# Optimization experiments

Measured on AMD Instinct MI355X. Metric: run time of the kernel, lower is better.

Reference implementation:

```python
import jax, jax.numpy as jnp
import numpy as np
from jax import lax

B, C, H, W = 16, 64, 64, 64
K = 3                  # kernel_size
D_IN = C * K           # moe input dim = 192
D_OUT = 128            # out_channels
N_EXP = 8
TOP_K = 2
N_SHARED = 1


def setup_inputs() -> dict:
    key = jax.random.key(0)
    ks = jax.random.split(key, 7)
    x = jax.random.normal(ks[0], (B, C, H, W), dtype=jnp.float32)
    # depthwise conv: groups=C, each input channel -> K output channels
    conv_w = jax.random.normal(ks[1], (D_IN, 1, K, K), dtype=jnp.float32) * 0.1
    router_w = jax.random.normal(ks[2], (D_IN, N_EXP), dtype=jnp.float32) * 0.05
    w_experts = jax.random.normal(ks[3], (N_EXP, D_IN, D_OUT), dtype=jnp.float32) * 0.05
    b_experts = jnp.zeros((N_EXP, D_OUT), dtype=jnp.float32)
    w_shared = jax.random.normal(ks[4], (N_SHARED, D_IN, D_OUT), dtype=jnp.float32) * 0.05
    b_shared = jnp.zeros((N_SHARED, D_OUT), dtype=jnp.float32)
    return {"x": x, "conv_w": conv_w, "router_w": router_w,
            "w_experts": w_experts, "b_experts": b_experts,
            "w_shared": w_shared, "b_shared": b_shared}


def _moe_conv2d(x, conv_w, router_w, w_experts, b_experts, w_shared, b_shared):
    pad = K // 2
    # depthwise conv (B,C,H,W) -> (B, C*K, H, W)
    x_conv = lax.conv_general_dilated(
        x, conv_w, window_strides=(1, 1), padding=[(pad, pad), (pad, pad)],
        feature_group_count=C, dimension_numbers=("NCHW", "OIHW", "NCHW"))
    # flatten to token stream (B*H*W, D_IN)
    tokens = x_conv.transpose(0, 2, 3, 1).reshape(-1, D_IN)
    # router: softmax probs, top-k gating renormalized over selected experts
    logits = tokens @ router_w                       # (T, E)
    probs = jax.nn.softmax(logits, axis=-1)
    top_v, top_i = lax.top_k(probs, TOP_K)           # (T, k)
    gates = top_v / jnp.sum(top_v, axis=-1, keepdims=True)
    # all-expert outputs then gather the selected k per token
    expert_out = jnp.einsum("ti,eio->teo", tokens, w_experts) + b_experts  # (T, E, O)
    sel = jnp.take_along_axis(expert_out, top_i[:, :, None], axis=1)       # (T, k, O)
    y_flat = jnp.einsum("tk,tko->to", gates, sel)
    # shared experts applied to every token
    shared = jnp.einsum("ti,sio->tso", tokens, w_shared) + b_shared        # (T, S, O)
    y_flat = y_flat + jnp.sum(shared, axis=1)
    # back to feature map (B, O, H, W)
    return y_flat.reshape(B, H, W, D_OUT).transpose(0, 3, 1, 2)


def reference(x, conv_w, router_w, w_experts, b_experts, w_shared, b_shared):
    return _moe_conv2d(x, conv_w, router_w, w_experts, b_experts, w_shared, b_shared)
```

## Files before the change

kernel.cpp:

```cpp
#include <hip/hip_runtime.h>
#include <math.h>

#define BB   16
#define CC   64
#define DIN  192
#define DOUT 128
#define NEXP 8
#define NMAT 9
#define NTOK 65536
#define CAP  65568
#define SLABROWS 65552

#define TOKSTRIDE 200
#define HALFSTRIDE 104
#define LOGSTRIDE 9
#define CSTRIDE 136

typedef short bf16x8 __attribute__((ext_vector_type(8)));
typedef float f32x4  __attribute__((ext_vector_type(4)));

#define WS_TOK   0u
#define WS_WT    25165824u
#define WS_CNT   25608192u
#define WS_RT    25608256u
#define WS_RG    27706432u
#define WS_SLAB  29804608u
#define WS_TOTAL  63367232u
#define WS_TOTAL3 80148544u
#define LPHALF 524288

__device__ __forceinline__ unsigned short f2bf(float f) {
    union { float f; unsigned u; } v; v.f = f;
    unsigned u = v.u;
    u += 0x7fffu + ((u >> 16) & 1u);
    return (unsigned short)(u >> 16);
}
__device__ __forceinline__ float bf2f(unsigned short s) {
    union { unsigned u; float f; } v; v.u = ((unsigned)s) << 16;
    return v.f;
}

__global__ __launch_bounds__(256)
void k1a_conv(const float* __restrict__ x,
              const float* __restrict__ conv_w,
              const float* __restrict__ router_w,
              unsigned short* __restrict__ tokbuf,
              float* __restrict__ lpart,
              int* __restrict__ cnt)
{
    __shared__ __attribute__((aligned(16))) unsigned short tokbf[64 * HALFSTRIDE];
    __shared__ float logits[64 * LOGSTRIDE];

    const int tid   = threadIdx.x;
    const int bid   = blockIdx.x;
    const int bh    = bid >> 1;
    const int chalf = bid & 1;
    const int b     = bh >> 6;
    const int h     = bh & 63;

    if (bid == 0 && tid < 16) cnt[tid] = 0;
    for (int idx = tid; idx < 64 * LOGSTRIDE; idx += 256) logits[idx] = 0.f;
    __syncthreads();

    const int   h0  = (h > 0)  ? (h - 1) : 0;
    const int   h2  = (h < 63) ? (h + 1) : 63;
    const float mh0 = (h > 0)  ? 1.f : 0.f;
    const float mh2 = (h < 63) ? 1.f : 0.f;

    const int w = tid & 63;
    const int q = __builtin_amdgcn_readfirstlane(tid >> 6);

    const int   wm  = (w == 0)  ? 0  : (w - 1);
    const int   wp  = (w == 63) ? 63 : (w + 1);
    const float mwm = (w == 0)  ? 0.f : 1.f;
    const float mwp = (w == 63) ? 0.f : 1.f;

    float lacc[8];
    #pragma unroll
    for (int e = 0; e < 8; ++e) lacc[e] = 0.f;

    const float* xb = x + (size_t)b * CC * 4096;

    #pragma unroll 2
    for (int i = 0; i < 8; ++i) {
        const int cl = q * 8 + i;
        const int c  = chalf * 32 + cl;
        const float* xc = xb + (size_t)c * 4096;
        const float* r0 = xc + h0 * 64;
        const float* r1 = xc + h  * 64;
        const float* r2 = xc + h2 * 64;
        float x00 = r0[wm], x01 = r0[w], x02 = r0[wp];
        float x10 = r1[wm], x11 = r1[w], x12 = r1[wp];
        float x20 = r2[wm], x21 = r2[w], x22 = r2[wp];
        x00 *= mh0 * mwm; x01 *= mh0; x02 *= mh0 * mwp;
        x10 *= mwm;                    x12 *= mwp;
        x20 *= mh2 * mwm; x21 *= mh2; x22 *= mh2 * mwp;

        #pragma unroll
        for (int j = 0; j < 3; ++j) {
            const int fl = 3 * cl + j;
            const int f  = chalf * 96 + fl;
            const float* w9 = conv_w + f * 9;
            float acc = x00 * w9[0] + x01 * w9[1] + x02 * w9[2]
                      + x10 * w9[3] + x11 * w9[4] + x12 * w9[5]
                      + x20 * w9[6] + x21 * w9[7] + x22 * w9[8];
            tokbf[w * HALFSTRIDE + fl] = f2bf(acc);
            const float* rwf = router_w + f * 8;
            #pragma unroll
            for (int e = 0; e < 8; ++e) lacc[e] += acc * rwf[e];
        }
    }

    #pragma unroll
    for (int e = 0; e < 8; ++e)
        atomicAdd(&logits[w * LOGSTRIDE + e], lacc[e]);
    __syncthreads();

    for (int idx = tid; idx < 512; idx += 256) {
        int wtok = idx >> 3, e = idx & 7;
        lpart[(size_t)chalf * LPHALF + ((size_t)bh * 64 + wtok) * 8 + e] =
            logits[wtok * LOGSTRIDE + e];
    }
    for (int idx = tid; idx < 768; idx += 256) {
        int row = idx / 12, seg = idx - row * 12;
        *(bf16x8*)(tokbuf + (size_t)(bh * 64 + row) * 192 + chalf * 96 + seg * 8) =
            *(const bf16x8*)(tokbf + row * HALFSTRIDE + seg * 8);
    }
}

__global__ __launch_bounds__(256)
void k1b_route(const float* __restrict__ lpart,
               int* __restrict__ cnt,
               int* __restrict__ rowtok, float* __restrict__ rowgate,
               const float* __restrict__ w_experts,
               const float* __restrict__ w_shared,
               unsigned short* __restrict__ wt)
{
    __shared__ int lcnt[8];
    __shared__ int lbase[8];

    const int tid = threadIdx.x;
    const int blk = blockIdx.x;
    const int t   = blk * 256 + tid;

    if (tid < 8) lcnt[tid] = 0;
    __syncthreads();

    const float* p0 = lpart + (size_t)t * 8;
    const float* p1 = lpart + LPHALF + (size_t)t * 8;
    float l[8];
    #pragma unroll
    for (int e = 0; e < 8; ++e) l[e] = p0[e] + p1[e];

    int e0 = 0; float l0 = l[0];
    #pragma unroll
    for (int e = 1; e < 8; ++e) if (l[e] > l0) { l0 = l[e]; e0 = e; }
    int e1 = -1; float l1 = -INFINITY;
    #pragma unroll
    for (int e = 0; e < 8; ++e) {
        if (e == e0) continue;
        if (l[e] > l1) { l1 = l[e]; e1 = e; }
    }
    float g0 = 1.f / (1.f + expf(l1 - l0));
    float g1 = 1.f - g0;

    int r0 = atomicAdd(&lcnt[e0], 1);
    int r1 = atomicAdd(&lcnt[e1], 1);
    __syncthreads();
    if (tid < 8) lbase[tid] = atomicAdd(&cnt[tid], lcnt[tid]);
    __syncthreads();

    int p0i = e0 * CAP + lbase[e0] + r0;
    int p1i = e1 * CAP + lbase[e1] + r1;
    rowtok[p0i]  = t;
    rowgate[p0i] = g0;
    rowtok[p1i]  = t | (1 << 20);
    rowgate[p1i] = g1;

    {
        int base = blk * 864;
        for (int q = 0; q < 4; ++q) {
            int idx = base + q * 256 + tid;
            if (idx < 221184 && (q * 256 + tid) < 864) {
                int e = idx / 24576, rem = idx - e * 24576;
                int n = rem / DIN,  k  = rem - n * DIN;
                const float* src = (e < 8) ? (w_experts + (size_t)e * DIN * DOUT)
                                           : w_shared;
                wt[idx] = f2bf(src[k * DOUT + n]);
            }
        }
    }
}

__global__ __launch_bounds__(256)
void k4_all(const unsigned short* __restrict__ tokbuf,
            const unsigned short* __restrict__ wt,
            const float* __restrict__ b_experts,
            const float* __restrict__ b_shared,
            const int* __restrict__ cnt,
            const int* __restrict__ rowtok, const float* __restrict__ rowgate,
            unsigned short* __restrict__ slab)
{
    __shared__ __attribute__((aligned(16))) unsigned short atile[2][16 * TOKSTRIDE];
    __shared__ __attribute__((aligned(16))) unsigned short ctile[2][16 * CSTRIDE];
    __shared__ int   stok[2][16];
    __shared__ float sgate[2][16];

    const int tid  = threadIdx.x;
    int e, jb, jstep;
    if (blockIdx.x < 2048) { e = blockIdx.x >> 8; jb = blockIdx.x & 255; jstep = 256; }
    else                   { e = 8; jb = blockIdx.x - 2048; jstep = 1024; }
    const bool dense = (e == 8);

    const int wave = tid >> 6;
    const int lane = tid & 63;
    const int m16  = lane & 15, quad = lane >> 4;
    const int o0   = (wave * 2 + 0) * 16 + m16;
    const int o1   = (wave * 2 + 1) * 16 + m16;

    const unsigned short* wb = wt + (size_t)e * DOUT * DIN;
    bf16x8 bfr0[6], bfr1[6];
    #pragma unroll
    for (int ks = 0; ks < 6; ++ks) {
        bfr0[ks] = *(const bf16x8*)(wb + (size_t)o0 * DIN + ks * 32 + quad * 8);
        bfr1[ks] = *(const bf16x8*)(wb + (size_t)o1 * DIN + ks * 32 + quad * 8);
    }
    const float be0 = dense ? b_shared[o0] : b_experts[e * DOUT + o0];
    const float be1 = dense ? b_shared[o1] : b_experts[e * DOUT + o1];

    const int cnt_e  = dense ? NTOK : cnt[e];
    const int ntiles = (cnt_e + 15) >> 4;
    const int*   rt = rowtok  + e * CAP;
    const float* rg = rowgate + e * CAP;

    const int r0i = tid / 24,         s0i = tid - r0i * 24;
    const int r1i = (tid + 256) / 24, s1i = (tid + 256) - r1i * 24;
    const bool has1 = (tid + 256) < 384;

    #define FETCH_RAW(r) (dense ? ((r) | (2 << 20)) : (((r) < cnt_e) ? rt[r] : NTOK))
    #define FETCH_G(r)   (dense ? 1.f : (((r) < cnt_e) ? rg[r] : 0.f))

    if (jb < ntiles) {
        int base = jb * 16;
        if (tid < 16) {
            stok[0][tid]  = FETCH_RAW(base + tid);
            sgate[0][tid] = FETCH_G(base + tid);
        }
        {
            int rawa = FETCH_RAW(base + r0i);
            *(bf16x8*)&atile[0][r0i * TOKSTRIDE + s0i * 8] =
                *(const bf16x8*)(tokbuf + (size_t)(rawa & 0x1FFFF) * 192 + s0i * 8);
            if (has1) {
                int rawb = FETCH_RAW(base + r1i);
                *(bf16x8*)&atile[0][r1i * TOKSTRIDE + s1i * 8] =
                    *(const bf16x8*)(tokbuf + (size_t)(rawb & 0x1FFFF) * 192 + s1i * 8);
            }
        }
    }
    __syncthreads();

    int buf = 0;
    for (int j = jb; j < ntiles; j += jstep, buf ^= 1) {
        const int jn = j + jstep;
        const bool more = (jn < ntiles);

        bf16x8 nx0 = {0,0,0,0,0,0,0,0}, nx1 = {0,0,0,0,0,0,0,0};
        int nmt = NTOK; float nmg = 0.f;
        if (more) {
            int base = jn * 16;
            if (tid < 16) { nmt = FETCH_RAW(base + tid); nmg = FETCH_G(base + tid); }
            int rawa = FETCH_RAW(base + r0i);
            nx0 = *(const bf16x8*)(tokbuf + (size_t)(rawa & 0x1FFFF) * 192 + s0i * 8);
            if (has1) {
                int rawb = FETCH_RAW(base + r1i);
                nx1 = *(const bf16x8*)(tokbuf + (size_t)(rawb & 0x1FFFF) * 192 + s1i * 8);
            }
        }

        bf16x8 a[6];
        #pragma unroll
        for (int ks = 0; ks < 6; ++ks)
            a[ks] = *(const bf16x8*)&atile[buf][m16 * TOKSTRIDE + ks * 32 + quad * 8];

        f32x4 acc0 = {0.f, 0.f, 0.f, 0.f};
        f32x4 acc1 = {0.f, 0.f, 0.f, 0.f};
        #pragma unroll
        for (int ks = 0; ks < 6; ++ks) {
            acc0 = __builtin_amdgcn_mfma_f32_16x16x32_bf16(a[ks], bfr0[ks], acc0, 0, 0, 0);
            acc1 = __builtin_amdgcn_mfma_f32_16x16x32_bf16(a[ks], bfr1[ks], acc1, 0, 0, 0);
        }

        #pragma unroll
        for (int i = 0; i < 4; ++i) {
            int   row = quad * 4 + i;
            float g   = sgate[buf][row];
            ctile[buf][row * CSTRIDE + o0] = f2bf(g * (acc0[i] + be0));
            ctile[buf][row * CSTRIDE + o1] = f2bf(g * (acc1[i] + be1));
        }

        if (more) {
            if (tid < 16) { stok[buf ^ 1][tid] = nmt; sgate[buf ^ 1][tid] = nmg; }
            *(bf16x8*)&atile[buf ^ 1][r0i * TOKSTRIDE + s0i * 8] = nx0;
            if (has1) *(bf16x8*)&atile[buf ^ 1][r1i * TOKSTRIDE + s1i * 8] = nx1;
        }
        __syncthreads();

        {
            int row = tid >> 4, chk = tid & 15;
            int raw = stok[buf][row];
            int t    = raw & 0x1FFFF;
            int slot = raw >> 20;
            *(bf16x8*)(slab + (size_t)slot * SLABROWS * DOUT
                            + (size_t)t * DOUT + chk * 8) =
                *(const bf16x8*)&ctile[buf][row * CSTRIDE + chk * 8];
        }
    }
    #undef FETCH_RAW
    #undef FETCH_G
}

__global__ __launch_bounds__(256)
void k3_combine(const unsigned short* __restrict__ slab,
                float* __restrict__ out)
{
    __shared__ float out_lds[32 * 129];

    const int tid = threadIdx.x;
    const int bid = blockIdx.x;
    const int bh  = bid >> 1;
    const int wh  = bid & 1;
    const int b   = bh >> 6;
    const int h   = bh & 63;
    const int t0  = bh * 64 + wh * 32;

    const unsigned short* s0 = slab;
    const unsigned short* s1 = slab + (size_t)SLABROWS * DOUT;
    const unsigned short* s2 = slab + (size_t)2 * SLABROWS * DOUT;

    #pragma unroll
    for (int it = 0; it < 2; ++it) {
        int idx = it * 256 + tid;
        int tl = idx >> 4, chk = idx & 15;
        size_t gt = (size_t)t0 + tl;
        bf16x8 v0 = *(const bf16x8*)(s0 + gt * DOUT + chk * 8);
        bf16x8 v1 = *(const bf16x8*)(s1 + gt * DOUT + chk * 8);
        bf16x8 v2 = *(const bf16x8*)(s2 + gt * DOUT + chk * 8);
        float* dst = &out_lds[tl * 129 + chk * 8];
        #pragma unroll
        for (int q = 0; q < 8; ++q)
            dst[q] = bf2f((unsigned short)v0[q]) + bf2f((unsigned short)v1[q])
                   + bf2f((unsigned short)v2[q]);
    }
    __syncthreads();

    float* outp = out + ((size_t)b * DOUT) * 4096 + h * 64 + wh * 32;
    for (int idx = tid; idx < 32 * DOUT; idx += 256) {
        int wloc = idx & 31, o = idx >> 5;
        outp[(size_t)o * 4096 + wloc] = out_lds[wloc * 129 + o];
    }
}

__global__ __launch_bounds__(256)
void k3_shared(const unsigned short* __restrict__ tokbuf,
               const unsigned short* __restrict__ wt,
               const unsigned short* __restrict__ slab,
               const float* __restrict__ b_shared,
               float* __restrict__ out)
{
    __shared__ float out_lds[32 * 129];

    const int tid  = threadIdx.x;
    const int bid  = blockIdx.x;
    const int bh   = bid >> 1;
    const int wh   = bid & 1;
    const int b    = bh >> 6;
    const int h    = bh & 63;
    const int wave = tid >> 6, lane = tid & 63;
    const int mt   = wave >> 1, nh = wave & 1;
    const int m16  = lane & 15, quad = lane >> 4;
    const int t0   = bh * 64 + wh * 32;

    bf16x8 pv0[2], pv1[2];
    {
        const unsigned short* s0 = slab;
        const unsigned short* s1 = slab + (size_t)SLABROWS * DOUT;
        #pragma unroll
        for (int it = 0; it < 2; ++it) {
            int idx = it * 256 + tid;
            int tl = idx >> 4, chk = idx & 15;
            size_t gt = (size_t)t0 + tl;
            pv0[it] = *(const bf16x8*)(s0 + gt * DOUT + chk * 8);
            pv1[it] = *(const bf16x8*)(s1 + gt * DOUT + chk * 8);
        }
    }

    const unsigned short* ap =
        tokbuf + (size_t)(t0 + mt * 16 + m16) * 192 + quad * 8;
    bf16x8 a[6];
    #pragma unroll
    for (int ks = 0; ks < 6; ++ks) a[ks] = *(const bf16x8*)(ap + ks * 32);

    const unsigned short* wsh = wt + (size_t)8 * DOUT * DIN;

    bf16x8 bcur[6], bnxt[6];
    {
        int o = (nh * 4 + 0) * 16 + m16;
        const unsigned short* bp = wsh + (size_t)o * DIN + quad * 8;
        #pragma unroll
        for (int ks = 0; ks < 6; ++ks) bcur[ks] = *(const bf16x8*)(bp + ks * 32);
    }
    #pragma unroll
    for (int nb2 = 0; nb2 < 4; ++nb2) {
        if (nb2 < 3) {
            int on = (nh * 4 + nb2 + 1) * 16 + m16;
            const unsigned short* bp = wsh + (size_t)on * DIN + quad * 8;
            #pragma unroll
            for (int ks = 0; ks < 6; ++ks) bnxt[ks] = *(const bf16x8*)(bp + ks * 32);
        }
        int o = (nh * 4 + nb2) * 16 + m16;
        f32x4 acc = {0.f, 0.f, 0.f, 0.f};
        #pragma unroll
        for (int ks = 0; ks < 6; ++ks)
            acc = __builtin_amdgcn_mfma_f32_16x16x32_bf16(a[ks], bcur[ks], acc, 0, 0, 0);
        float bs = b_shared[o];
        #pragma unroll
        for (int i = 0; i < 4; ++i) {
            int tloc = mt * 16 + quad * 4 + i;
            out_lds[tloc * 129 + o] = acc[i] + bs;
        }
        #pragma unroll
        for (int ks = 0; ks < 6; ++ks) bcur[ks] = bnxt[ks];
    }
    __syncthreads();

    #pragma unroll
    for (int it = 0; it < 2; ++it) {
        int idx = it * 256 + tid;
        int tl = idx >> 4, chk = idx & 15;
        float* dst = &out_lds[tl * 129 + chk * 8];
        #pragma unroll
        for (int q = 0; q < 8; ++q)
            dst[q] += bf2f((unsigned short)pv0[it][q])
                    + bf2f((unsigned short)pv1[it][q]);
    }
    __syncthreads();

    float* outp = out + ((size_t)b * DOUT) * 4096 + h * 64 + wh * 32;
    for (int idx = tid; idx < 32 * DOUT; idx += 256) {
        int wloc = idx & 31, o = idx >> 5;
        outp[(size_t)o * 4096 + wloc] = out_lds[wloc * 129 + o];
    }
}

#define OUTSTRIDE 129
#define MAXROWS 320
#define MAXTILES 20

__global__ __launch_bounds__(256)
void moe_conv2d_mfma(const float* __restrict__ x,
                     const float* __restrict__ conv_w,
                     const float* __restrict__ router_w,
                     const unsigned short* __restrict__ wt,
                     const float* __restrict__ b_experts,
                     const float* __restrict__ b_shared,
                     float* __restrict__ out)
{
    __shared__ __attribute__((aligned(16))) unsigned short tokbf[64 * TOKSTRIDE];
    __shared__ float out_lds[64 * OUTSTRIDE];
    __shared__ float rw[DIN * NEXP];
    __shared__ float logits[64 * LOGSTRIDE];
    __shared__ float sg0[64], sg1[64];
    __shared__ int   se0[64], se1[64];
    __shared__ int   rowtok[MAXROWS];
    __shared__ float rowgate[MAXROWS];
    __shared__ int   cbuf[NMAT];
    __shared__ int   tilexp[MAXTILES], tilebase[MAXTILES];
    __shared__ int   ntiles_s;

    const int tid = threadIdx.x;
    const int bh  = blockIdx.x;
    const int b   = bh >> 6;
    const int h   = bh & 63;

    for (int idx = tid; idx < DIN * NEXP; idx += 256) rw[idx] = router_w[idx];
    for (int idx = tid; idx < 64 * LOGSTRIDE; idx += 256) logits[idx] = 0.f;
    __syncthreads();
    {
        const int w  = tid & 63;
        const int fq = tid >> 6;
        float lacc[8];
        #pragma unroll
        for (int e = 0; e < 8; ++e) lacc[e] = 0.f;
        for (int i = 0; i < 48; ++i) {
            int f = i * 4 + fq;
            int c = f / 3;
            const float* wp    = conv_w + f * 9;
            const float* xbase = x + ((size_t)(b * 64 + c) * 64) * 64;
            float acc = 0.f;
            #pragma unroll
            for (int kh = 0; kh < 3; ++kh) {
                int hh = h + kh - 1;
                if (hh < 0 || hh > 63) continue;
                const float* xrow = xbase + hh * 64;
                #pragma unroll
                for (int kw = 0; kw < 3; ++kw) {
                    int ww = w + kw - 1;
                    if (ww < 0 || ww > 63) continue;
                    acc += xrow[ww] * wp[kh * 3 + kw];
                }
            }
            tokbf[w * TOKSTRIDE + f] = f2bf(acc);
            const float* rwf = rw + f * 8;
            #pragma unroll
            for (int e = 0; e < 8; ++e) lacc[e] += acc * rwf[e];
        }
        #pragma unroll
        for (int e = 0; e < 8; ++e)
            atomicAdd(&logits[w * LOGSTRIDE + e], lacc[e]);
    }
    __syncthreads();
    if (tid < 64) {
        int w = tid;
        float l[8];
        #pragma unroll
        for (int e = 0; e < 8; ++e) l[e] = logits[w * LOGSTRIDE + e];
        int e0 = 0; float l0 = l[0];
        #pragma unroll
        for (int e = 1; e < 8; ++e) if (l[e] > l0) { l0 = l[e]; e0 = e; }
        int e1 = -1; float l1 = -INFINITY;
        #pragma unroll
        for (int e = 0; e < 8; ++e) {
            if (e == e0) continue;
            if (l[e] > l1) { l1 = l[e]; e1 = e; }
        }
        float g0 = 1.f / (1.f + expf(l1 - l0));
        sg0[w] = g0; sg1[w] = 1.f - g0;
        se0[w] = e0; se1[w] = e1;
    }
    __syncthreads();
    for (int idx = tid; idx < 64 * DOUT; idx += 256) {
        int t = idx >> 7, o = idx & 127;
        out_lds[t * OUTSTRIDE + o] = b_shared[o]
            + sg0[t] * b_experts[se0[t] * DOUT + o]
            + sg1[t] * b_experts[se1[t] * DOUT + o];
    }
    if (tid < 8) {
        int c = 0;
        for (int t = 0; t < 64; ++t) c += (se0[t] == tid) + (se1[t] == tid);
        cbuf[tid] = c;
    } else if (tid == 8) cbuf[8] = 64;
    __syncthreads();
    if (tid < NMAT) {
        int e = tid;
        int start = 0, tb = 0;
        for (int e2 = 0; e2 < e; ++e2) {
            int ce = cbuf[e2];
            int tl = (ce + 15) >> 4;
            start += tl << 4; tb += tl;
        }
        int ce = cbuf[e];
        int tl = (ce + 15) >> 4;
        for (int j = 0; j < tl; ++j) { tilexp[tb + j] = e; tilebase[tb + j] = start + (j << 4); }
        if (e == 8) ntiles_s = tb + tl;
        int j = 0;
        if (e < 8) {
            for (int t = 0; t < 64; ++t) {
                if (se0[t] == e) { rowtok[start + j] = t; rowgate[start + j] = sg0[t]; ++j; }
                if (se1[t] == e) { rowtok[start + j] = t; rowgate[start + j] = sg1[t]; ++j; }
            }
        } else {
            for (int t = 0; t < 64; ++t) { rowtok[start + j] = t; rowgate[start + j] = 1.f; ++j; }
        }
        for (; j < (tl << 4); ++j) { rowtok[start + j] = 0; rowgate[start + j] = 0.f; }
    }
    __syncthreads();
    {
        const int wave = tid >> 6;
        const int lane = tid & 63;
        const int m16  = lane & 15;
        const int quad = lane >> 4;
        const int nt   = ntiles_s;
        for (int ti = wave; ti < nt; ti += 4) {
            int e    = tilexp[ti];
            int base = tilebase[ti];
            int tA = rowtok[base + m16];
            bf16x8 a[6];
            #pragma unroll
            for (int ks = 0; ks < 6; ++ks)
                a[ks] = *(const bf16x8*)(tokbf + tA * TOKSTRIDE + ks * 32 + quad * 8);
            int st[4]; float sgt[4];
            #pragma unroll
            for (int i2 = 0; i2 < 4; ++i2) {
                int r = base + quad * 4 + i2;
                st[i2] = rowtok[r]; sgt[i2] = rowgate[r];
            }
            const unsigned short* we = wt + (size_t)e * DOUT * DIN;
            for (int n = 0; n < 8; ++n) {
                const unsigned short* wp = we + (size_t)(n * 16 + m16) * DIN + quad * 8;
                f32x4 acc = {0.f, 0.f, 0.f, 0.f};
                #pragma unroll
                for (int ks = 0; ks < 6; ++ks) {
                    bf16x8 bfr2 = *(const bf16x8*)(wp + ks * 32);
                    acc = __builtin_amdgcn_mfma_f32_16x16x32_bf16(a[ks], bfr2, acc, 0, 0, 0);
                }
                int ncol = n * 16 + m16;
                #pragma unroll
                for (int i2 = 0; i2 < 4; ++i2)
                    atomicAdd(&out_lds[st[i2] * OUTSTRIDE + ncol], sgt[i2] * acc[i2]);
            }
        }
    }
    __syncthreads();
    {
        float* outp = out + (((size_t)b * DOUT) * 64 + h) * 64;
        for (int idx = tid; idx < 64 * DOUT; idx += 256) {
            int w = idx & 63, o = idx >> 6;
            outp[(size_t)o * 4096 + w] = out_lds[w * OUTSTRIDE + o];
        }
    }
}

__global__ __launch_bounds__(256)
void prep_weights_only(const float* __restrict__ w_experts,
                       const float* __restrict__ w_shared,
                       unsigned short* __restrict__ wt)
{
    int e = blockIdx.x;
    const float* src = (e < 8) ? (w_experts + (size_t)e * DIN * DOUT) : w_shared;
    unsigned short* dst = wt + (size_t)e * DOUT * DIN;
    for (int idx = threadIdx.x; idx < DOUT * DIN; idx += 256) {
        int n = idx / DIN, k = idx - n * DIN;
        dst[idx] = f2bf(src[k * DOUT + n]);
    }
}

extern "C" void kernel_launch(void* const* d_in, const int* in_sizes, int n_in,
                              void* d_out, int out_size, void* d_ws, size_t ws_size,
                              hipStream_t stream)
{
    const float* x         = (const float*)d_in[0];
    const float* conv_w    = (const float*)d_in[1];
    const float* router_w  = (const float*)d_in[2];
    const float* w_experts = (const float*)d_in[3];
    const float* b_experts = (const float*)d_in[4];
    const float* w_shared  = (const float*)d_in[5];
    const float* b_shared  = (const float*)d_in[6];
    float* out = (float*)d_out;
    char* ws = (char*)d_ws;

    if (ws_size >= WS_TOTAL) {
        unsigned short* tokbuf  = (unsigned short*)(ws + WS_TOK);
        unsigned short* wt      = (unsigned short*)(ws + WS_WT);
        int*            cnt     = (int*)(ws + WS_CNT);
        int*            rowtok  = (int*)(ws + WS_RT);
        float*          rowgate = (float*)(ws + WS_RG);
        unsigned short* slab    = (unsigned short*)(ws + WS_SLAB);
        float*          lpart   = (float*)(ws + WS_SLAB);

        k1a_conv<<<dim3(2048), dim3(256), 0, stream>>>(
            x, conv_w, router_w, tokbuf, lpart, cnt);
        k1b_route<<<dim3(256), dim3(256), 0, stream>>>(
            lpart, cnt, rowtok, rowgate, w_experts, w_shared, wt);
        if (ws_size >= WS_TOTAL3) {
            k4_all<<<dim3(3072), dim3(256), 0, stream>>>(
                tokbuf, wt, b_experts, b_shared, cnt, rowtok, rowgate, slab);
            k3_combine<<<dim3(2048), dim3(256), 0, stream>>>(slab, out);
        } else {
            k4_all<<<dim3(2048), dim3(256), 0, stream>>>(
                tokbuf, wt, b_experts, b_shared, cnt, rowtok, rowgate, slab);
            k3_shared<<<dim3(2048), dim3(256), 0, stream>>>(
                tokbuf, wt, slab, b_shared, out);
        }
    } else {
        unsigned short* wt = (unsigned short*)ws;
        prep_weights_only<<<dim3(NMAT), dim3(256), 0, stream>>>(w_experts, w_shared, wt);
        moe_conv2d_mfma<<<dim3(1024), dim3(256), 0, stream>>>(
            x, conv_w, router_w, wt, b_experts, b_shared, out);
    }
}
```

Baseline: 165.4 us.

## Fuse routing and weight conversion into conv kernel, one block per row

Each conv block now handles all 64 channels of one image row instead of half, so full router logits are available locally and top-2 routing plus row-slot assignment happen in the same kernel. This removes the separate routing kernel, the partial-logit round trip through global memory and one launch, and the weight transpose/bf16 conversion is spread across the conv blocks. The counter reset moves to a memset. In exchange the grid is halved, so each block does twice the conv work with a larger LDS tile, which lowers parallelism.

```diff
diff --git a/kernel.cpp b/kernel.cpp
--- a/kernel.cpp
+++ b/kernel.cpp
@@ -12,7 +12,6 @@
 #define SLABROWS 65552
 
 #define TOKSTRIDE 200
-#define HALFSTRIDE 104
 #define LOGSTRIDE 9
 #define CSTRIDE 136
 
@@ -27,7 +26,6 @@
 #define WS_SLAB  29804608u
 #define WS_TOTAL  63367232u
 #define WS_TOTAL3 80148544u
-#define LPHALF 524288
 
 __device__ __forceinline__ unsigned short f2bf(float f) {
     union { float f; unsigned u; } v; v.f = f;
@@ -44,23 +42,37 @@
 void k1a_conv(const float* __restrict__ x,
               const float* __restrict__ conv_w,
               const float* __restrict__ router_w,
+              const float* __restrict__ w_experts,
+              const float* __restrict__ w_shared,
               unsigned short* __restrict__ tokbuf,
-              float* __restrict__ lpart,
-              int* __restrict__ cnt)
+              unsigned short* __restrict__ wt,
+              int* __restrict__ cnt,
+              int* __restrict__ rowtok, float* __restrict__ rowgate)
 {
-    __shared__ __attribute__((aligned(16))) unsigned short tokbf[64 * HALFSTRIDE];
+    __shared__ __attribute__((aligned(16))) unsigned short tokbf[64 * TOKSTRIDE];
     __shared__ float logits[64 * LOGSTRIDE];
-
-    const int tid   = threadIdx.x;
-    const int bid   = blockIdx.x;
-    const int bh    = bid >> 1;
-    const int chalf = bid & 1;
-    const int b     = bh >> 6;
-    const int h     = bh & 63;
-
-    if (bid == 0 && tid < 16) cnt[tid] = 0;
+    __shared__ int lcnt[8];
+    __shared__ int lbase[8];
+
+    const int tid = threadIdx.x;
+    const int bh  = blockIdx.x;
+    const int b   = bh >> 6;
+    const int h   = bh & 63;
+
     for (int idx = tid; idx < 64 * LOGSTRIDE; idx += 256) logits[idx] = 0.f;
-    __syncthreads();
+    if (tid < 8) lcnt[tid] = 0;
+    __syncthreads();
+
+    {
+        int idx = bh * 216 + tid;
+        if (tid < 216) {
+            int e = idx / 24576, rem = idx - e * 24576;
+            int n = rem / DIN,  k  = rem - n * DIN;
+            const float* src = (e < 8) ? (w_experts + (size_t)e * DIN * DOUT)
+                                       : w_shared;
+            wt[idx] = f2bf(src[k * DOUT + n]);
+        }
+    }
 
     const int   h0  = (h > 0)  ? (h - 1) : 0;
     const int   h2  = (h < 63) ? (h + 1) : 63;
@@ -82,9 +94,8 @@
     const float* xb = x + (size_t)b * CC * 4096;
 
     #pragma unroll 2
-    for (int i = 0; i < 8; ++i) {
-        const int cl = q * 8 + i;
-        const int c  = chalf * 32 + cl;
+    for (int i = 0; i < 16; ++i) {
+        const int c = q * 16 + i;
         const float* xc = xb + (size_t)c * 4096;
         const float* r0 = xc + h0 * 64;
         const float* r1 = xc + h  * 64;
@@ -98,14 +109,13 @@
 
         #pragma unroll
         for (int j = 0; j < 3; ++j) {
-            const int fl = 3 * cl + j;
-            const int f  = chalf * 96 + fl;
-            const float* w9 = conv_w + f * 9;
+            const int f = 3 * c + j;
+            const float* w9  = conv_w + f * 9;
+            const float* rwf = router_w + f * 8;
             float acc = x00 * w9[0] + x01 * w9[1] + x02 * w9[2]
                       + x10 * w9[3] + x11 * w9[4] + x12 * w9[5]
                       + x20 * w9[6] + x21 * w9[7] + x22 * w9[8];
-            tokbf[w * HALFSTRIDE + fl] = f2bf(acc);
-            const float* rwf = router_w + f * 8;
+            tokbf[w * TOKSTRIDE + f] = f2bf(acc);
             #pragma unroll
             for (int e = 0; e < 8; ++e) lacc[e] += acc * rwf[e];
         }
@@ -116,79 +126,43 @@
         atomicAdd(&logits[w * LOGSTRIDE + e], lacc[e]);
     __syncthreads();
 
-    for (int idx = tid; idx < 512; idx += 256) {
-        int wtok = idx >> 3, e = idx & 7;
-        lpart[(size_t)chalf * LPHALF + ((size_t)bh * 64 + wtok) * 8 + e] =
-            logits[wtok * LOGSTRIDE + e];
-    }
-    for (int idx = tid; idx < 768; idx += 256) {
-        int row = idx / 12, seg = idx - row * 12;
-        *(bf16x8*)(tokbuf + (size_t)(bh * 64 + row) * 192 + chalf * 96 + seg * 8) =
-            *(const bf16x8*)(tokbf + row * HALFSTRIDE + seg * 8);
-    }
-}
-
-__global__ __launch_bounds__(256)
-void k1b_route(const float* __restrict__ lpart,
-               int* __restrict__ cnt,
-               int* __restrict__ rowtok, float* __restrict__ rowgate,
-               const float* __restrict__ w_experts,
-               const float* __restrict__ w_shared,
-               unsigned short* __restrict__ wt)
-{
-    __shared__ int lcnt[8];
-    __shared__ int lbase[8];
-
-    const int tid = threadIdx.x;
-    const int blk = blockIdx.x;
-    const int t   = blk * 256 + tid;
-
-    if (tid < 8) lcnt[tid] = 0;
-    __syncthreads();
-
-    const float* p0 = lpart + (size_t)t * 8;
-    const float* p1 = lpart + LPHALF + (size_t)t * 8;
-    float l[8];
-    #pragma unroll
-    for (int e = 0; e < 8; ++e) l[e] = p0[e] + p1[e];
-
-    int e0 = 0; float l0 = l[0];
-    #pragma unroll
-    for (int e = 1; e < 8; ++e) if (l[e] > l0) { l0 = l[e]; e0 = e; }
-    int e1 = -1; float l1 = -INFINITY;
-    #pragma unroll
-    for (int e = 0; e < 8; ++e) {
-        if (e == e0) continue;
-        if (l[e] > l1) { l1 = l[e]; e1 = e; }
-    }
-    float g0 = 1.f / (1.f + expf(l1 - l0));
-    float g1 = 1.f - g0;
-
-    int r0 = atomicAdd(&lcnt[e0], 1);
-    int r1 = atomicAdd(&lcnt[e1], 1);
+    int e0 = 0, e1 = -1, r0k = 0, r1k = 0;
+    float g0 = 0.f, g1 = 0.f;
+    if (tid < 64) {
+        float l[8];
+        #pragma unroll
+        for (int e = 0; e < 8; ++e) l[e] = logits[tid * LOGSTRIDE + e];
+        float l0 = l[0];
+        #pragma unroll
+        for (int e = 1; e < 8; ++e) if (l[e] > l0) { l0 = l[e]; e0 = e; }
+        float l1 = -INFINITY;
+        #pragma unroll
+        for (int e = 0; e < 8; ++e) {
+            if (e == e0) continue;
+            if (l[e] > l1) { l1 = l[e]; e1 = e; }
+        }
+        g0 = 1.f / (1.f + expf(l1 - l0));
+        g1 = 1.f - g0;
+        r0k = atomicAdd(&lcnt[e0], 1);
+        r1k = atomicAdd(&lcnt[e1], 1);
+    }
     __syncthreads();
     if (tid < 8) lbase[tid] = atomicAdd(&cnt[tid], lcnt[tid]);
     __syncthreads();
-
-    int p0i = e0 * CAP + lbase[e0] + r0;
-    int p1i = e1 * CAP + lbase[e1] + r1;
-    rowtok[p0i]  = t;
-    rowgate[p0i] = g0;
-    rowtok[p1i]  = t | (1 << 20);
-    rowgate[p1i] = g1;
-
-    {
-        int base = blk * 864;
-        for (int q = 0; q < 4; ++q) {
-            int idx = base + q * 256 + tid;
-            if (idx < 221184 && (q * 256 + tid) < 864) {
-                int e = idx / 24576, rem = idx - e * 24576;
-                int n = rem / DIN,  k  = rem - n * DIN;
-                const float* src = (e < 8) ? (w_experts + (size_t)e * DIN * DOUT)
-                                           : w_shared;
-                wt[idx] = f2bf(src[k * DOUT + n]);
-            }
-        }
+    if (tid < 64) {
+        int t   = bh * 64 + tid;
+        int p0i = e0 * CAP + lbase[e0] + r0k;
+        int p1i = e1 * CAP + lbase[e1] + r1k;
+        rowtok[p0i]  = t;
+        rowgate[p0i] = g0;
+        rowtok[p1i]  = t | (1 << 20);
+        rowgate[p1i] = g1;
+    }
+
+    for (int idx = tid; idx < 1536; idx += 256) {
+        int row = idx / 24, seg = idx - row * 24;
+        *(bf16x8*)(tokbuf + (size_t)(bh * 64 + row) * 192 + seg * 8) =
+            *(const bf16x8*)(tokbf + row * TOKSTRIDE + seg * 8);
     }
 }
 
@@ -655,12 +629,11 @@
         int*            rowtok  = (int*)(ws + WS_RT);
         float*          rowgate = (float*)(ws + WS_RG);
         unsigned short* slab    = (unsigned short*)(ws + WS_SLAB);
-        float*          lpart   = (float*)(ws + WS_SLAB);
-
-        k1a_conv<<<dim3(2048), dim3(256), 0, stream>>>(
-            x, conv_w, router_w, tokbuf, lpart, cnt);
-        k1b_route<<<dim3(256), dim3(256), 0, stream>>>(
-            lpart, cnt, rowtok, rowgate, w_experts, w_shared, wt);
+
+        hipMemsetAsync(cnt, 0, 16 * sizeof(int), stream);
+        k1a_conv<<<dim3(1024), dim3(256), 0, stream>>>(
+            x, conv_w, router_w, w_experts, w_shared,
+            tokbuf, wt, cnt, rowtok, rowgate);
         if (ws_size >= WS_TOTAL3) {
             k4_all<<<dim3(3072), dim3(256), 0, stream>>>(
                 tokbuf, wt, b_experts, b_shared, cnt, rowtok, rowgate, slab);
```

Result: faster. 159.7 us (-3.4%).
